# Optimization experiments

Measured on AMD Instinct MI355X. Metric: run time of the kernel, lower is better.

The kernel has to match this reference:

```python
import jax, jax.numpy as jnp
import numpy as np

B, D, C = 8192, 2048, 1000

def setup_inputs() -> dict:
    key = jax.random.key(0)
    k1, k2, k3 = jax.random.split(key, 3)
    x = jax.random.normal(k1, (B, D), dtype=jnp.float32)
    W = jax.random.normal(k2, (D, C), dtype=jnp.float32) * (1.0 / np.sqrt(D))
    b = jax.random.normal(k3, (C,), dtype=jnp.float32) * 0.01
    return {"x": x, "W": W, "b": b}

def reference(x, W, b):
    # inner classifier: logits out[b, c]
    out = jnp.dot(x, W) + b  # [B, C]
    # leave-one-out logsumexp per class, fused:
    # lse_k = logsumexp(out[:, != k]) = lse_all + log1p(-exp(out_k - lse_all))
    lse = jax.nn.logsumexp(out, axis=1, keepdims=True)  # [B, 1]
    loo = lse + jnp.log1p(-jnp.exp(out - lse))           # [B, C]
    # c_out = -loo; return c_out + out
    return out - loo
```

## Files before the change

kernel.cpp:

```cpp
#include <hip/hip_runtime.h>
#include <hip/hip_bf16.h>
#include <math.h>

#define BDIM 8192
#define DDIM 2048
#define CDIM 1000
#define NPAD 1024
#define BK   64

#define WS_XB_BYTES   33554432ULL
#define WS_BT_BYTES    4194304ULL
#define WS_C1_OFFSET  37748736ULL
#define WS_NEED       70516736ULL

typedef __attribute__((ext_vector_type(8))) short short8;
typedef __attribute__((ext_vector_type(4))) float floatx4;

__device__ __forceinline__ unsigned short f2bf(float f) {
    union { float f; unsigned u; } a; a.f = f;
    unsigned u = a.u;
    u = (u + 0x7fff + ((u >> 16) & 1)) >> 16;
    return (unsigned short)u;
}

__device__ __forceinline__ void async_copy16(const void* gp, void* lp) {
    __builtin_amdgcn_global_load_lds(
        (const __attribute__((address_space(1))) void*)gp,
        (__attribute__((address_space(3))) void*)lp,
        16, 0, 0);
}

__global__ __launch_bounds__(256) void cvt_kernel(
    const float* __restrict__ x, unsigned short* __restrict__ xb,
    const float* __restrict__ W, unsigned short* __restrict__ Bt)
{
    const int blk = blockIdx.x;
    const int t   = threadIdx.x;
    if (blk < 16384) {
        int i = blk * 256 + t;
        float4 v = ((const float4*)x)[i];
        ushort4 o;
        o.x = f2bf(v.x); o.y = f2bf(v.y); o.z = f2bf(v.z); o.w = f2bf(v.w);
        ((ushort4*)xb)[i] = o;
    } else {
        __shared__ float tile[32][33];
        const int b2 = blk - 16384;
        const int k0 = (b2 & 63) * 32;
        const int n0 = (b2 >> 6) * 32;
        const int tx = t & 31, ty = t >> 5;
        #pragma unroll
        for (int i = 0; i < 4; i++) {
            int k = k0 + ty + i * 8;
            int n = n0 + tx;
            tile[ty + i * 8][tx] = (n < CDIM) ? W[(size_t)k * CDIM + n] : 0.0f;
        }
        __syncthreads();
        #pragma unroll
        for (int i = 0; i < 4; i++) {
            int n = n0 + ty + i * 8;
            int k = k0 + tx;
            Bt[(size_t)n * DDIM + k] = f2bf(tile[tx][ty + i * 8]);
        }
    }
}

__device__ __forceinline__ void gemm_body(
    const unsigned short* __restrict__ A,
    const unsigned short* __restrict__ Bt,
    float* __restrict__ C,
    int mBase, int nBase, int kBase, int kIters,
    unsigned short* As, unsigned short* Bs)
{
    const int t    = threadIdx.x;
    const int wave = t >> 6;
    const int lane = t & 63;
    const int wm   = wave & 1;
    const int wn   = wave >> 1;
    const int quad = lane >> 4;
    const int l16  = lane & 15;

    floatx4 acc[4][4] = {};

    const int byteoff = t * 16;
    const int rowA    = byteoff >> 7;
    const int colb    = byteoff & 127;
    const char* Ag = (const char*)A  + ((size_t)(mBase + rowA) * DDIM + kBase) * 2 + colb;
    const char* Bg = (const char*)Bt + ((size_t)(nBase + rowA) * DDIM + kBase) * 2 + colb;
    char* AsDst = (char*)As + byteoff;
    char* BsDst = (char*)Bs + byteoff;

    for (int kt = 0; kt < kIters * BK; kt += BK) {
        const char* a = Ag + kt * 2;
        const char* b = Bg + kt * 2;
        #pragma unroll
        for (int r = 0; r < 4; r++) {
            async_copy16(a + (size_t)r * 32 * DDIM * 2, AsDst + r * 4096);
            async_copy16(b + (size_t)r * 32 * DDIM * 2, BsDst + r * 4096);
        }
        __syncthreads();

        #pragma unroll
        for (int ks = 0; ks < 2; ks++) {
            short8 af[4], bfr[4];
            #pragma unroll
            for (int mi = 0; mi < 4; mi++)
                af[mi] = *(const short8*)(As + (wm * 64 + mi * 16 + l16) * BK + ks * 32 + quad * 8);
            #pragma unroll
            for (int ni = 0; ni < 4; ni++)
                bfr[ni] = *(const short8*)(Bs + (wn * 64 + ni * 16 + l16) * BK + ks * 32 + quad * 8);
            #pragma unroll
            for (int mi = 0; mi < 4; mi++)
                #pragma unroll
                for (int ni = 0; ni < 4; ni++)
                    acc[mi][ni] = __builtin_amdgcn_mfma_f32_16x16x32_bf16(
                        af[mi], bfr[ni], acc[mi][ni], 0, 0, 0);
        }
        __syncthreads();
    }

    #pragma unroll
    for (int mi = 0; mi < 4; mi++) {
        int row0 = mBase + wm * 64 + mi * 16 + quad * 4;
        #pragma unroll
        for (int ni = 0; ni < 4; ni++) {
            int col = nBase + wn * 64 + ni * 16 + l16;
            if (col < CDIM) {
                #pragma unroll
                for (int rg = 0; rg < 4; rg++)
                    C[(size_t)(row0 + rg) * CDIM + col] = acc[mi][ni][rg];
            }
        }
    }
}

__global__ __launch_bounds__(256, 4) void gemm_splitk_kernel(
    const unsigned short* __restrict__ A,
    const unsigned short* __restrict__ Bt,
    float* __restrict__ C0, float* __restrict__ C1)
{
    __shared__ unsigned short As[128 * BK];
    __shared__ unsigned short Bs[128 * BK];

    const int L   = blockIdx.x;
    const int xcd = L & 7;
    const int s   = L >> 3;
    const int mz  = xcd * 16 + (s >> 3);
    const int n_t = s & 7;
    const int m_t = mz >> 1;
    const int z   = mz & 1;

    float* C = z ? C1 : C0;
    gemm_body(A, Bt, C, m_t * 128, n_t * 128, z * (DDIM / 2), (DDIM / 2) / BK, As, Bs);
}

__global__ __launch_bounds__(256, 2) void gemm_single_kernel(
    const unsigned short* __restrict__ A,
    const unsigned short* __restrict__ Bt,
    float* __restrict__ C0)
{
    __shared__ unsigned short As[128 * BK];
    __shared__ unsigned short Bs[128 * BK];

    const int L   = blockIdx.x;
    const int xcd = L & 7;
    const int s   = L >> 3;
    const int m_t = xcd * 8 + (s >> 3);
    const int n_t = s & 7;

    gemm_body(A, Bt, C0, m_t * 128, n_t * 128, 0, DDIM / BK, As, Bs);
}

__global__ __launch_bounds__(256) void lse_kernel(
    float* __restrict__ C, const float* C1,
    const float* __restrict__ bias, int split)
{
    const int row = blockIdx.x;
    const int t   = threadIdx.x;
    __shared__ float red[8];

    const bool valid = t < (CDIM / 4);
    const int c0 = t * 4;

    float4 v = make_float4(-INFINITY, -INFINITY, -INFINITY, -INFINITY);
    if (valid) {
        v = *(const float4*)(C + (size_t)row * CDIM + c0);
        if (split) {
            float4 p = *(const float4*)(C1 + (size_t)row * CDIM + c0);
            v.x += p.x; v.y += p.y; v.z += p.z; v.w += p.w;
        }
        float4 bb = *(const float4*)(bias + c0);
        v.x += bb.x; v.y += bb.y; v.z += bb.z; v.w += bb.w;
    }

    float m = fmaxf(fmaxf(v.x, v.y), fmaxf(v.z, v.w));
    #pragma unroll
    for (int off = 32; off > 0; off >>= 1)
        m = fmaxf(m, __shfl_down(m, off, 64));
    const int wave = t >> 6;
    if ((t & 63) == 0) red[wave] = m;
    __syncthreads();
    if (t == 0) red[4] = fmaxf(fmaxf(red[0], red[1]), fmaxf(red[2], red[3]));
    __syncthreads();
    const float M = red[4];

    float4 e = make_float4(0.f, 0.f, 0.f, 0.f);
    float s = 0.f;
    if (valid) {
        e.x = expf(v.x - M); e.y = expf(v.y - M);
        e.z = expf(v.z - M); e.w = expf(v.w - M);
        s = e.x + e.y + e.z + e.w;
    }
    #pragma unroll
    for (int off = 32; off > 0; off >>= 1)
        s += __shfl_down(s, off, 64);
    if ((t & 63) == 0) red[wave] = s;
    __syncthreads();
    if (t == 0) red[4] = red[0] + red[1] + red[2] + red[3];
    __syncthreads();
    const float S    = red[4];
    const float lse  = M + logf(S);
    const float invS = 1.0f / S;

    if (valid) {
        float4 o;
        o.x = (v.x - lse) - log1pf(-e.x * invS);
        o.y = (v.y - lse) - log1pf(-e.y * invS);
        o.z = (v.z - lse) - log1pf(-e.z * invS);
        o.w = (v.w - lse) - log1pf(-e.w * invS);
        *(float4*)(C + (size_t)row * CDIM + c0) = o;
    }
}

extern "C" void kernel_launch(void* const* d_in, const int* in_sizes, int n_in,
                              void* d_out, int out_size, void* d_ws, size_t ws_size,
                              hipStream_t stream) {
    const float* x = (const float*)d_in[0];
    const float* W = (const float*)d_in[1];
    const float* b = (const float*)d_in[2];
    float* out = (float*)d_out;

    unsigned short* xb = (unsigned short*)d_ws;
    unsigned short* Bt = xb + (size_t)BDIM * DDIM;
    float* C1 = (float*)((char*)d_ws + WS_C1_OFFSET);
    const bool splitk = ws_size >= WS_NEED;

    cvt_kernel<<<18432, 256, 0, stream>>>(x, xb, W, Bt);

    if (splitk) {
        gemm_splitk_kernel<<<1024, 256, 0, stream>>>(xb, Bt, out, C1);
        lse_kernel<<<BDIM, 256, 0, stream>>>(out, C1, b, 1);
    } else {
        gemm_single_kernel<<<512, 256, 0, stream>>>(xb, Bt, out);
        lse_kernel<<<BDIM, 256, 0, stream>>>(out, nullptr, b, 0);
    }
}
```

Measured before the change: 184.2 us.

## Fuse x fp32-to-bf16 conversion into GEMM A-tile loads

Removes the separate pass that converts x to bf16 in workspace. The GEMM now reads fp32 x directly, converts it in registers with a round-half-up perm trick and stores it to LDS, while only W is pre-converted. This saves a full write and re-read of a 32MB bf16 copy of x, but the GEMM now reads twice the A bytes per tile through synchronous loads instead of async LDS copies. The rounding also changes from round-to-nearest-even to round-half-up, and the workspace requirement shrinks.

```diff
diff --git a/kernel.cpp b/kernel.cpp
--- a/kernel.cpp
+++ b/kernel.cpp
@@ -8,10 +8,8 @@
 #define NPAD 1024
 #define BK   64
 
-#define WS_XB_BYTES   33554432ULL
-#define WS_BT_BYTES    4194304ULL
-#define WS_C1_OFFSET  37748736ULL
-#define WS_NEED       70516736ULL
+#define WS_C1_OFFSET  4194304ULL
+#define WS_NEED      36962304ULL
 
 typedef __attribute__((ext_vector_type(8))) short short8;
 typedef __attribute__((ext_vector_type(4))) float floatx4;
@@ -30,42 +28,43 @@
         16, 0, 0);
 }
 
-__global__ __launch_bounds__(256) void cvt_kernel(
-    const float* __restrict__ x, unsigned short* __restrict__ xb,
+__device__ __forceinline__ void cvt8_store(float4 a, float4 b, unsigned short* dst) {
+    union { float4 v; unsigned u[4]; } ua, ub;
+    ua.v = a; ub.v = b;
+    unsigned d0 = __builtin_amdgcn_perm(ua.u[1] + 0x8000u, ua.u[0] + 0x8000u, 0x07060302u);
+    unsigned d1 = __builtin_amdgcn_perm(ua.u[3] + 0x8000u, ua.u[2] + 0x8000u, 0x07060302u);
+    unsigned d2 = __builtin_amdgcn_perm(ub.u[1] + 0x8000u, ub.u[0] + 0x8000u, 0x07060302u);
+    unsigned d3 = __builtin_amdgcn_perm(ub.u[3] + 0x8000u, ub.u[2] + 0x8000u, 0x07060302u);
+    uint4 o; o.x = d0; o.y = d1; o.z = d2; o.w = d3;
+    *(uint4*)dst = o;
+}
+
+__global__ __launch_bounds__(256) void cvt_w_kernel(
     const float* __restrict__ W, unsigned short* __restrict__ Bt)
 {
-    const int blk = blockIdx.x;
-    const int t   = threadIdx.x;
-    if (blk < 16384) {
-        int i = blk * 256 + t;
-        float4 v = ((const float4*)x)[i];
-        ushort4 o;
-        o.x = f2bf(v.x); o.y = f2bf(v.y); o.z = f2bf(v.z); o.w = f2bf(v.w);
-        ((ushort4*)xb)[i] = o;
-    } else {
-        __shared__ float tile[32][33];
-        const int b2 = blk - 16384;
-        const int k0 = (b2 & 63) * 32;
-        const int n0 = (b2 >> 6) * 32;
-        const int tx = t & 31, ty = t >> 5;
-        #pragma unroll
-        for (int i = 0; i < 4; i++) {
-            int k = k0 + ty + i * 8;
-            int n = n0 + tx;
-            tile[ty + i * 8][tx] = (n < CDIM) ? W[(size_t)k * CDIM + n] : 0.0f;
-        }
-        __syncthreads();
-        #pragma unroll
-        for (int i = 0; i < 4; i++) {
-            int n = n0 + ty + i * 8;
-            int k = k0 + tx;
-            Bt[(size_t)n * DDIM + k] = f2bf(tile[tx][ty + i * 8]);
-        }
+    __shared__ float tile[32][33];
+    const int b2 = blockIdx.x;
+    const int k0 = (b2 & 63) * 32;
+    const int n0 = (b2 >> 6) * 32;
+    const int t  = threadIdx.x;
+    const int tx = t & 31, ty = t >> 5;
+    #pragma unroll
+    for (int i = 0; i < 4; i++) {
+        int k = k0 + ty + i * 8;
+        int n = n0 + tx;
+        tile[ty + i * 8][tx] = (n < CDIM) ? W[(size_t)k * CDIM + n] : 0.0f;
+    }
+    __syncthreads();
+    #pragma unroll
+    for (int i = 0; i < 4; i++) {
+        int n = n0 + ty + i * 8;
+        int k = k0 + tx;
+        Bt[(size_t)n * DDIM + k] = f2bf(tile[tx][ty + i * 8]);
     }
 }
 
 __device__ __forceinline__ void gemm_body(
-    const unsigned short* __restrict__ A,
+    const float* __restrict__ A,
     const unsigned short* __restrict__ Bt,
     float* __restrict__ C,
     int mBase, int nBase, int kBase, int kIters,
@@ -82,20 +81,28 @@
     floatx4 acc[4][4] = {};
 
     const int byteoff = t * 16;
-    const int rowA    = byteoff >> 7;
+    const int rowB    = byteoff >> 7;
     const int colb    = byteoff & 127;
-    const char* Ag = (const char*)A  + ((size_t)(mBase + rowA) * DDIM + kBase) * 2 + colb;
-    const char* Bg = (const char*)Bt + ((size_t)(nBase + rowA) * DDIM + kBase) * 2 + colb;
-    char* AsDst = (char*)As + byteoff;
+    const char* Bg = (const char*)Bt + ((size_t)(nBase + rowB) * DDIM + kBase) * 2 + colb;
     char* BsDst = (char*)Bs + byteoff;
 
+    const int ar = t >> 3;
+    const int ac = (t & 7) * 8;
+    const float* Ag = A + (size_t)(mBase + ar) * DDIM + kBase + ac;
+    unsigned short* AsW = As + ar * BK + ac;
+
     for (int kt = 0; kt < kIters * BK; kt += BK) {
-        const char* a = Ag + kt * 2;
         const char* b = Bg + kt * 2;
         #pragma unroll
+        for (int r = 0; r < 4; r++)
+            async_copy16(b + (size_t)r * 32 * DDIM * 2, BsDst + r * 4096);
+
+        const float* a = Ag + kt;
+        #pragma unroll
         for (int r = 0; r < 4; r++) {
-            async_copy16(a + (size_t)r * 32 * DDIM * 2, AsDst + r * 4096);
-            async_copy16(b + (size_t)r * 32 * DDIM * 2, BsDst + r * 4096);
+            float4 v0 = *(const float4*)(a + (size_t)r * 32 * DDIM);
+            float4 v1 = *(const float4*)(a + (size_t)r * 32 * DDIM + 4);
+            cvt8_store(v0, v1, AsW + r * 32 * BK);
         }
         __syncthreads();
 
@@ -134,7 +141,7 @@
 }
 
 __global__ __launch_bounds__(256, 4) void gemm_splitk_kernel(
-    const unsigned short* __restrict__ A,
+    const float* __restrict__ A,
     const unsigned short* __restrict__ Bt,
     float* __restrict__ C0, float* __restrict__ C1)
 {
@@ -153,8 +160,8 @@
     gemm_body(A, Bt, C, m_t * 128, n_t * 128, z * (DDIM / 2), (DDIM / 2) / BK, As, Bs);
 }
 
-__global__ __launch_bounds__(256, 2) void gemm_single_kernel(
-    const unsigned short* __restrict__ A,
+__global__ __launch_bounds__(256, 4) void gemm_single_kernel(
+    const float* __restrict__ A,
     const unsigned short* __restrict__ Bt,
     float* __restrict__ C0)
 {
@@ -182,6 +189,7 @@
     const int c0 = t * 4;
 
     float4 v = make_float4(-INFINITY, -INFINITY, -INFINITY, -INFINITY);
+    float4 e = make_float4(0.f, 0.f, 0.f, 0.f);
     if (valid) {
         v = *(const float4*)(C + (size_t)row * CDIM + c0);
         if (split) {
@@ -203,7 +211,6 @@
     __syncthreads();
     const float M = red[4];
 
-    float4 e = make_float4(0.f, 0.f, 0.f, 0.f);
     float s = 0.f;
     if (valid) {
         e.x = expf(v.x - M); e.y = expf(v.y - M);
@@ -239,18 +246,17 @@
     const float* b = (const float*)d_in[2];
     float* out = (float*)d_out;
 
-    unsigned short* xb = (unsigned short*)d_ws;
-    unsigned short* Bt = xb + (size_t)BDIM * DDIM;
+    unsigned short* Bt = (unsigned short*)d_ws;
     float* C1 = (float*)((char*)d_ws + WS_C1_OFFSET);
     const bool splitk = ws_size >= WS_NEED;
 
-    cvt_kernel<<<18432, 256, 0, stream>>>(x, xb, W, Bt);
+    cvt_w_kernel<<<2048, 256, 0, stream>>>(W, Bt);
 
     if (splitk) {
-        gemm_splitk_kernel<<<1024, 256, 0, stream>>>(xb, Bt, out, C1);
+        gemm_splitk_kernel<<<1024, 256, 0, stream>>>(x, Bt, out, C1);
         lse_kernel<<<BDIM, 256, 0, stream>>>(out, C1, b, 1);
     } else {
-        gemm_single_kernel<<<512, 256, 0, stream>>>(xb, Bt, out);
+        gemm_single_kernel<<<512, 256, 0, stream>>>(x, Bt, out);
         lse_kernel<<<BDIM, 256, 0, stream>>>(out, nullptr, b, 0);
     }
 }
```

Result: slower. 229.5 us (+24.6%).

## Load A fragments directly from global and double-buffer B tiles in LDS

Applied to the files above, without the earlier changes.

The GEMM body no longer stages the A (x) tile through LDS. Each wave reads its A fragments straight from global memory into registers. B tiles are double-buffered in LDS, so the next tile's async copy is issued while the current one is consumed, which removes one barrier per iteration. This aims to overlap loads with MFMA work and cut LDS traffic. The cost is uncoalesced, latency-exposed global reads for A that are repeated across the wn waves, plus higher launch bounds on the single-pass kernel.

```diff
diff --git a/kernel.cpp b/kernel.cpp
--- a/kernel.cpp
+++ b/kernel.cpp
@@ -8,8 +8,6 @@
 #define NPAD 1024
 #define BK   64
 
-#define WS_XB_BYTES   33554432ULL
-#define WS_BT_BYTES    4194304ULL
 #define WS_C1_OFFSET  37748736ULL
 #define WS_NEED       70516736ULL
 
@@ -69,7 +67,7 @@
     const unsigned short* __restrict__ Bt,
     float* __restrict__ C,
     int mBase, int nBase, int kBase, int kIters,
-    unsigned short* As, unsigned short* Bs)
+    unsigned short* Bs)
 {
     const int t    = threadIdx.x;
     const int wave = t >> 6;
@@ -82,32 +80,41 @@
     floatx4 acc[4][4] = {};
 
     const int byteoff = t * 16;
-    const int rowA    = byteoff >> 7;
+    const int rowB    = byteoff >> 7;
     const int colb    = byteoff & 127;
-    const char* Ag = (const char*)A  + ((size_t)(mBase + rowA) * DDIM + kBase) * 2 + colb;
-    const char* Bg = (const char*)Bt + ((size_t)(nBase + rowA) * DDIM + kBase) * 2 + colb;
-    char* AsDst = (char*)As + byteoff;
-    char* BsDst = (char*)Bs + byteoff;
-
-    for (int kt = 0; kt < kIters * BK; kt += BK) {
-        const char* a = Ag + kt * 2;
-        const char* b = Bg + kt * 2;
-        #pragma unroll
-        for (int r = 0; r < 4; r++) {
-            async_copy16(a + (size_t)r * 32 * DDIM * 2, AsDst + r * 4096);
-            async_copy16(b + (size_t)r * 32 * DDIM * 2, BsDst + r * 4096);
-        }
+    const char* Bg = (const char*)Bt + ((size_t)(nBase + rowB) * DDIM + kBase) * 2 + colb;
+    char* Dst0 = (char*)Bs + byteoff;
+    char* Dst1 = (char*)Bs + 16384 + byteoff;
+
+    const unsigned short* Ab = A + (size_t)(mBase + wm * 64 + l16) * DDIM + kBase + quad * 8;
+
+    #pragma unroll
+    for (int r = 0; r < 4; r++)
+        async_copy16(Bg + (size_t)r * 32 * DDIM * 2, Dst0 + r * 4096);
+
+    for (int i = 0; i < kIters; i++) {
         __syncthreads();
+
+        if (i + 1 < kIters) {
+            const char* bnext = Bg + (size_t)(i + 1) * BK * 2;
+            char* dst = ((i + 1) & 1) ? Dst1 : Dst0;
+            #pragma unroll
+            for (int r = 0; r < 4; r++)
+                async_copy16(bnext + (size_t)r * 32 * DDIM * 2, dst + r * 4096);
+        }
+
+        const unsigned short* Bcur = Bs + ((i & 1) ? 8192 : 0);
+        const unsigned short* Ai   = Ab + i * BK;
 
         #pragma unroll
         for (int ks = 0; ks < 2; ks++) {
             short8 af[4], bfr[4];
             #pragma unroll
             for (int mi = 0; mi < 4; mi++)
-                af[mi] = *(const short8*)(As + (wm * 64 + mi * 16 + l16) * BK + ks * 32 + quad * 8);
+                af[mi] = *(const short8*)(Ai + (size_t)mi * 16 * DDIM + ks * 32);
             #pragma unroll
             for (int ni = 0; ni < 4; ni++)
-                bfr[ni] = *(const short8*)(Bs + (wn * 64 + ni * 16 + l16) * BK + ks * 32 + quad * 8);
+                bfr[ni] = *(const short8*)(Bcur + (wn * 64 + ni * 16 + l16) * BK + ks * 32 + quad * 8);
             #pragma unroll
             for (int mi = 0; mi < 4; mi++)
                 #pragma unroll
@@ -115,7 +122,6 @@
                     acc[mi][ni] = __builtin_amdgcn_mfma_f32_16x16x32_bf16(
                         af[mi], bfr[ni], acc[mi][ni], 0, 0, 0);
         }
-        __syncthreads();
     }
 
     #pragma unroll
@@ -138,8 +144,7 @@
     const unsigned short* __restrict__ Bt,
     float* __restrict__ C0, float* __restrict__ C1)
 {
-    __shared__ unsigned short As[128 * BK];
-    __shared__ unsigned short Bs[128 * BK];
+    __shared__ unsigned short Bs[2 * 128 * BK];
 
     const int L   = blockIdx.x;
     const int xcd = L & 7;
@@ -150,16 +155,15 @@
     const int z   = mz & 1;
 
     float* C = z ? C1 : C0;
-    gemm_body(A, Bt, C, m_t * 128, n_t * 128, z * (DDIM / 2), (DDIM / 2) / BK, As, Bs);
-}
-
-__global__ __launch_bounds__(256, 2) void gemm_single_kernel(
+    gemm_body(A, Bt, C, m_t * 128, n_t * 128, z * (DDIM / 2), (DDIM / 2) / BK, Bs);
+}
+
+__global__ __launch_bounds__(256, 4) void gemm_single_kernel(
     const unsigned short* __restrict__ A,
     const unsigned short* __restrict__ Bt,
     float* __restrict__ C0)
 {
-    __shared__ unsigned short As[128 * BK];
-    __shared__ unsigned short Bs[128 * BK];
+    __shared__ unsigned short Bs[2 * 128 * BK];
 
     const int L   = blockIdx.x;
     const int xcd = L & 7;
@@ -167,7 +171,7 @@
     const int m_t = xcd * 8 + (s >> 3);
     const int n_t = s & 7;
 
-    gemm_body(A, Bt, C0, m_t * 128, n_t * 128, 0, DDIM / BK, As, Bs);
+    gemm_body(A, Bt, C0, m_t * 128, n_t * 128, 0, DDIM / BK, Bs);
 }
 
 __global__ __launch_bounds__(256) void lse_kernel(
@@ -182,6 +186,7 @@
     const int c0 = t * 4;
 
     float4 v = make_float4(-INFINITY, -INFINITY, -INFINITY, -INFINITY);
+    float4 e = make_float4(0.f, 0.f, 0.f, 0.f);
     if (valid) {
         v = *(const float4*)(C + (size_t)row * CDIM + c0);
         if (split) {
@@ -203,7 +208,6 @@
     __syncthreads();
     const float M = red[4];
 
-    float4 e = make_float4(0.f, 0.f, 0.f, 0.f);
     float s = 0.f;
     if (valid) {
         e.x = expf(v.x - M); e.y = expf(v.y - M);
```

After: 215.9 us. +17.2%, slower.
